# Optimization experiments

Hardware: AMD Instinct MI355X
Metric: run time of the kernel (lower is better)

Reference implementation:

```python
import jax, jax.numpy as jnp
import numpy as np

N_NODES = 100000
N_EDGES = 1600000
D_IN = 64
D_HID = 64
D_OUT = 64


def setup_inputs() -> dict:
    key = jax.random.key(0)
    ks = jax.random.split(key, 12)
    x = jax.random.normal(ks[0], (N_NODES, D_IN), dtype=jnp.float32)
    edge_index = jax.random.randint(ks[1], (2, N_EDGES), 0, N_NODES, dtype=jnp.int64)
    batch = jnp.zeros((N_NODES,), dtype=jnp.int64)
    # Glorot-ish init for GCNConv weights; PyG stores weight as [in, out] applied as x @ W.
    def lin(k, din, dout):
        s = 1.0 / np.sqrt(din)
        return jax.random.uniform(k, (din, dout), minval=-s, maxval=s, dtype=jnp.float32)
    W1 = lin(ks[2], D_IN, D_HID);  b1 = jnp.zeros((D_HID,), jnp.float32)
    W2 = lin(ks[3], D_HID, D_HID); b2 = jnp.zeros((D_HID,), jnp.float32)
    W3 = lin(ks[4], D_HID, D_HID); b3 = jnp.zeros((D_HID,), jnp.float32)
    W4 = lin(ks[5], D_HID, D_OUT); b4 = jnp.zeros((D_OUT,), jnp.float32)
    return {"x": x, "edge_index": edge_index, "batch": batch,
            "W1": W1, "b1": b1, "W2": W2, "b2": b2,
            "W3": W3, "b3": b3, "W4": W4, "b4": b4}


def reference(x, edge_index, batch, W1, b1, W2, b2, W3, b3, W4, b4):
    N = x.shape[0]
    loops = jnp.arange(N, dtype=edge_index.dtype)
    src = jnp.concatenate([edge_index[0], loops])  # [E+N]
    dst = jnp.concatenate([edge_index[1], loops])  # [E+N]
    # Symmetric normalization: deg over A + I (in-degree at dst), norm_e = d_src^-1/2 * d_dst^-1/2
    deg = jax.ops.segment_sum(jnp.ones(src.shape, dtype=x.dtype), dst, num_segments=N)
    dis = jnp.where(deg > 0, jax.lax.rsqrt(deg), 0.0)
    norm = (dis[src] * dis[dst])[:, None]  # [E+N, 1]

    def conv(h, W, b):
        h = h @ W                                   # [N, dout]
        msg = h[src] * norm                         # gather + scale, [E+N, dout]
        return jax.ops.segment_sum(msg, dst, num_segments=N) + b

    h = jax.nn.elu(conv(x, W1, b1))   # dropout_p=0.0 -> identity
    h = jax.nn.elu(conv(h, W2, b2))
    h = jax.nn.elu(conv(h, W3, b3))
    return conv(h, W4, b4)
```

## Files before the change

kernel.cpp:

```cpp
#include <hip/hip_runtime.h>

#define NN 100000
#define NE 1600000
#define DD 64
#define BSH 9
#define BSZ 512
#define NBKT 196
#define CHUNK 8192
#define NCH ((NE + CHUNK - 1) / CHUNK)
#define CSR2_CAP (NE + 16 * (NBKT * BSZ))


__global__ __launch_bounds__(256) void k_bcount(const int* __restrict__ ei,
                                                int* __restrict__ bcnt) {
    __shared__ int h[NBKT];
    int t = threadIdx.x;
    for (int i = t; i < NBKT; i += 256) h[i] = 0;
    __syncthreads();
    int base = blockIdx.x * CHUNK;
    for (int i = t; i < CHUNK; i += 256) {
        int e = base + i;
        if (e < NE) atomicAdd(&h[ei[NE + e] >> BSH], 1);
    }
    __syncthreads();
    for (int i = t; i < NBKT; i += 256)
        if (h[i]) atomicAdd(&bcnt[i], h[i]);
}


__global__ __launch_bounds__(256) void k_bscan(const int* __restrict__ bcnt,
                                               int* __restrict__ bbase,
                                               int* __restrict__ bcur) {
    __shared__ int s[256];
    int t = threadIdx.x;
    int v = (t < NBKT) ? bcnt[t] : 0;
    s[t] = v;
    __syncthreads();
    for (int o = 1; o < 256; o <<= 1) {
        int x = (t >= o) ? s[t - o] : 0;
        __syncthreads();
        s[t] += x;
        __syncthreads();
    }
    int ex = s[t] - v;
    if (t < NBKT) { bbase[t] = ex; bcur[t] = ex; }
    if (t == NBKT) bbase[NBKT] = ex;
}


__global__ __launch_bounds__(256) void k_bscat(const int* __restrict__ ei,
                                               int* __restrict__ bcur,
                                               int* __restrict__ bkt) {
    __shared__ int h[NBKT], rbase[NBKT], rcur[NBKT];
    int t = threadIdx.x;
    for (int i = t; i < NBKT; i += 256) h[i] = 0;
    __syncthreads();
    int cb = blockIdx.x * CHUNK;
    int s[32], d[32];
#pragma unroll
    for (int i = 0; i < 32; ++i) {
        int e = cb + t + 256 * i;
        if (e < NE) {
            s[i] = ei[e];
            d[i] = ei[NE + e];
            atomicAdd(&h[d[i] >> BSH], 1);
        } else {
            d[i] = -1;
        }
    }
    __syncthreads();
    for (int i = t; i < NBKT; i += 256) {
        int c = h[i];
        rbase[i] = c ? atomicAdd(&bcur[i], c) : 0;
        rcur[i] = 0;
    }
    __syncthreads();
#pragma unroll
    for (int i = 0; i < 32; ++i) {
        if (d[i] >= 0) {
            int b = d[i] >> BSH;
            int pos = rbase[b] + atomicAdd(&rcur[b], 1);
            bkt[pos] = s[i] | ((d[i] & (BSZ - 1)) << 17);
        }
    }
}


__global__ __launch_bounds__(256) void k_ncnt(const int* __restrict__ bbase,
                                              const int* __restrict__ bkt,
                                              int* __restrict__ ncnt,
                                              int* __restrict__ bptot,
                                              double* __restrict__ dis) {
    __shared__ int cnt[BSZ];
    __shared__ int red[256];
    int b = blockIdx.x, t = threadIdx.x;
    cnt[t] = 0; cnt[t + 256] = 0;
    __syncthreads();
    int beg = bbase[b], end = bbase[b + 1];
    for (int j = beg + t; j < end; j += 256)
        atomicAdd(&cnt[bkt[j] >> 17], 1);
    __syncthreads();
    int nb = b * BSZ;
    int n0 = nb + t, n1 = nb + t + 256;
    int c0 = cnt[t], c1 = cnt[t + 256];
    int p0 = (n0 < NN) ? ((c0 + 16) & ~15) : 0;
    int p1 = (n1 < NN) ? ((c1 + 16) & ~15) : 0;
    if (n0 < NN) { ncnt[n0] = c0; dis[n0] = 1.0 / sqrt((double)(c0 + 1)); }
    if (n1 < NN) { ncnt[n1] = c1; dis[n1] = 1.0 / sqrt((double)(c1 + 1)); }
    red[t] = p0 + p1;
    __syncthreads();
    for (int o = 128; o > 0; o >>= 1) {
        if (t < o) red[t] += red[t + o];
        __syncthreads();
    }
    if (t == 0) bptot[b] = red[0];
}


__global__ __launch_bounds__(256) void k_pscan(const int* __restrict__ bptot,
                                               int* __restrict__ pbase,
                                               int* __restrict__ rp2) {
    __shared__ int s[256];
    int t = threadIdx.x;
    int v = (t < NBKT) ? bptot[t] : 0;
    s[t] = v;
    __syncthreads();
    for (int o = 1; o < 256; o <<= 1) {
        int x = (t >= o) ? s[t - o] : 0;
        __syncthreads();
        s[t] += x;
        __syncthreads();
    }
    int ex = s[t] - v;
    if (t < NBKT) pbase[t] = ex;
    if (t == NBKT) rp2[NN] = ex;
}


__global__ __launch_bounds__(256) void k_bfill(const int* __restrict__ bbase,
                                               const int* __restrict__ bkt,
                                               const int* __restrict__ ncnt,
                                               const int* __restrict__ pbase,
                                               int* __restrict__ rp2,
                                               int* __restrict__ csr2) {
    __shared__ int cur[BSZ];
    __shared__ int s2[256];
    int b = blockIdx.x, t = threadIdx.x;
    int nb = b * BSZ;
    int gbase = pbase[b];
    int n0 = nb + 2 * t, n1 = nb + 2 * t + 1;
    int c0 = (n0 < NN) ? ncnt[n0] : -1;
    int c1 = (n1 < NN) ? ncnt[n1] : -1;
    int q0 = (c0 >= 0) ? ((c0 + 16) & ~15) : 0;
    int q1 = (c1 >= 0) ? ((c1 + 16) & ~15) : 0;
    s2[t] = q0 + q1;
    __syncthreads();
    for (int o = 1; o < 256; o <<= 1) {
        int v = (t >= o) ? s2[t - o] : 0;
        __syncthreads();
        s2[t] += v;
        __syncthreads();
    }
    int ex = s2[t] - (q0 + q1);
    if (c0 >= 0) { int g = gbase + ex;      rp2[n0] = g; csr2[g] = n0; cur[2 * t]     = ex + 1; }
    if (c1 >= 0) { int g = gbase + ex + q0; rp2[n1] = g; csr2[g] = n1; cur[2 * t + 1] = ex + q0 + 1; }
    __syncthreads();
    int beg = bbase[b], end = bbase[b + 1];
    for (int j = beg + t; j < end; j += 256) {
        int pk = bkt[j];
        int pos = gbase + atomicAdd(&cur[pk >> 17], 1);
        csr2[pos] = pk & 0x1FFFF;
    }
    __syncthreads();
    if (c0 >= 0) { int e0 = ex + q0;      for (int j = cur[2 * t];     j < e0; ++j) csr2[gbase + j] = NN; }
    if (c1 >= 0) { int e1 = ex + q0 + q1; for (int j = cur[2 * t + 1]; j < e1; ++j) csr2[gbase + j] = NN; }
}


__global__ __launch_bounds__(256) void k_gemm(const float* __restrict__ in,
                                              const float* __restrict__ W,
                                              const double* __restrict__ dis,
                                              float* __restrict__ h2s) {
    __shared__ float sW[DD * DD];
    __shared__ float sIn[128 * 65];
    int t = threadIdx.x;
    int brow = blockIdx.x * 128;
#pragma unroll
    for (int i = 0; i < 16; ++i) sW[t + 256 * i] = W[t + 256 * i];
#pragma unroll
    for (int i = 0; i < 32; ++i) {
        int idx = t + 256 * i;
        int rr = idx >> 6, kk = idx & 63;
        int gr = brow + rr; if (gr >= NN) gr = NN - 1;
        sIn[rr * 65 + kk] = in[(size_t)gr * DD + kk];
    }
    __syncthreads();
    int cg = t & 7;
    int rg = t >> 3;
    const float* sInB = &sIn[rg * 4 * 65];

    float aE[4][8], aO[4][8];
#pragma unroll
    for (int i = 0; i < 4; ++i)
#pragma unroll
        for (int j = 0; j < 8; ++j) { aE[i][j] = 0.f; aO[i][j] = 0.f; }

#pragma unroll 4
    for (int k = 0; k < DD; k += 2) {
        float4 w0 = *(const float4*)&sW[k * DD + cg * 8];
        float4 w1 = *(const float4*)&sW[k * DD + cg * 8 + 4];
        float4 w2 = *(const float4*)&sW[(k + 1) * DD + cg * 8];
        float4 w3 = *(const float4*)&sW[(k + 1) * DD + cg * 8 + 4];
        float wv0[8] = {w0.x, w0.y, w0.z, w0.w, w1.x, w1.y, w1.z, w1.w};
        float wv1[8] = {w2.x, w2.y, w2.z, w2.w, w3.x, w3.y, w3.z, w3.w};
#pragma unroll
        for (int i = 0; i < 4; ++i) {
            float a0 = sInB[i * 65 + k];
            float a1 = sInB[i * 65 + k + 1];
#pragma unroll
            for (int j = 0; j < 8; ++j) {
                aE[i][j] = fmaf(a0, wv0[j], aE[i][j]);
                aO[i][j] = fmaf(a1, wv1[j], aO[i][j]);
            }
        }
    }

#pragma unroll
    for (int i = 0; i < 4; ++i) {
        int row = brow + rg * 4 + i;
        if (row < NN) {
            double dr = dis[row];
            float o[8];
#pragma unroll
            for (int j = 0; j < 8; ++j)
                o[j] = (float)((double)(aE[i][j] + aO[i][j]) * dr);
            *(float4*)&h2s[(size_t)row * DD + cg * 8]     = make_float4(o[0], o[1], o[2], o[3]);
            *(float4*)&h2s[(size_t)row * DD + cg * 8 + 4] = make_float4(o[4], o[5], o[6], o[7]);
        }
    }
}


__global__ __launch_bounds__(256) void k_aggr(const int* __restrict__ rp2,
                                              const int* __restrict__ csr2,
                                              const float* __restrict__ h2s,
                                              const double* __restrict__ dis,
                                              const float* __restrict__ b,
                                              float* __restrict__ out,
                                              int apply_elu) {
    int gid = blockIdx.x * 256 + threadIdx.x;
    int node = gid >> 6;
    int lane = gid & 63;
    int beg = __builtin_amdgcn_readfirstlane(rp2[node]);
    int end = __builtin_amdgcn_readfirstlane(rp2[node + 1]);
    double a0 = 0.0, a1 = 0.0, a2 = 0.0, a3 = 0.0;
    for (int j = beg; j < end; j += 16) {
        int4 i0 = *(const int4*)&csr2[j];
        int4 i1 = *(const int4*)&csr2[j + 4];
        int4 i2 = *(const int4*)&csr2[j + 8];
        int4 i3 = *(const int4*)&csr2[j + 12];
        float v0  = h2s[(size_t)(unsigned)i0.x * DD + lane];
        float v1  = h2s[(size_t)(unsigned)i0.y * DD + lane];
        float v2  = h2s[(size_t)(unsigned)i0.z * DD + lane];
        float v3  = h2s[(size_t)(unsigned)i0.w * DD + lane];
        float v4  = h2s[(size_t)(unsigned)i1.x * DD + lane];
        float v5  = h2s[(size_t)(unsigned)i1.y * DD + lane];
        float v6  = h2s[(size_t)(unsigned)i1.z * DD + lane];
        float v7  = h2s[(size_t)(unsigned)i1.w * DD + lane];
        float v8  = h2s[(size_t)(unsigned)i2.x * DD + lane];
        float v9  = h2s[(size_t)(unsigned)i2.y * DD + lane];
        float v10 = h2s[(size_t)(unsigned)i2.z * DD + lane];
        float v11 = h2s[(size_t)(unsigned)i2.w * DD + lane];
        float v12 = h2s[(size_t)(unsigned)i3.x * DD + lane];
        float v13 = h2s[(size_t)(unsigned)i3.y * DD + lane];
        float v14 = h2s[(size_t)(unsigned)i3.z * DD + lane];
        float v15 = h2s[(size_t)(unsigned)i3.w * DD + lane];
        a0 += (double)v0;  a1 += (double)v1;  a2 += (double)v2;  a3 += (double)v3;
        a0 += (double)v4;  a1 += (double)v5;  a2 += (double)v6;  a3 += (double)v7;
        a0 += (double)v8;  a1 += (double)v9;  a2 += (double)v10; a3 += (double)v11;
        a0 += (double)v12; a1 += (double)v13; a2 += (double)v14; a3 += (double)v15;
    }
    double sum = (a0 + a1) + (a2 + a3);
    float vf = (float)(dis[node] * sum + (double)b[lane]);
    if (apply_elu && vf <= 0.f) vf = expm1f(vf);
    out[gid] = vf;
}


static inline size_t align256(size_t x) { return (x + 255) & ~(size_t)255; }

extern "C" void kernel_launch(void* const* d_in, const int* in_sizes, int n_in,
                              void* d_out, int out_size, void* d_ws, size_t ws_size,
                              hipStream_t stream) {
    const float* x  = (const float*)d_in[0];
    const int*   ei = (const int*)d_in[1];
    const float* W1 = (const float*)d_in[3];
    const float* b1 = (const float*)d_in[4];
    const float* W2 = (const float*)d_in[5];
    const float* b2 = (const float*)d_in[6];
    const float* W3 = (const float*)d_in[7];
    const float* b3 = (const float*)d_in[8];
    const float* W4 = (const float*)d_in[9];
    const float* b4 = (const float*)d_in[10];
    float* out = (float*)d_out;

    char* ws = (char*)d_ws;
    size_t off = 0;
    double* dis   = (double*)(ws + off); off = align256(off + (size_t)NN * sizeof(double));
    float*  h2s   = (float*) (ws + off); off = align256(off + (size_t)(NN + 1) * DD * sizeof(float));
    float*  A     = (float*) (ws + off); off = align256(off + (size_t)NN * DD * sizeof(float));
    int*    ncnt  = (int*)   (ws + off); off = align256(off + (size_t)NN * sizeof(int));
    int*    rp2   = (int*)   (ws + off); off = align256(off + (size_t)(NN + 1) * sizeof(int));
    int*    bcnt  = (int*)   (ws + off); off = align256(off + (size_t)(NBKT + 1) * sizeof(int));
    int*    bbase = (int*)   (ws + off); off = align256(off + (size_t)(NBKT + 1) * sizeof(int));
    int*    bcur  = (int*)   (ws + off); off = align256(off + (size_t)(NBKT + 1) * sizeof(int));
    int*    bptot = (int*)   (ws + off); off = align256(off + (size_t)(NBKT + 1) * sizeof(int));
    int*    pbase = (int*)   (ws + off); off = align256(off + (size_t)(NBKT + 1) * sizeof(int));
    int*    bkt   = (int*)   (ws + off); off = align256(off + (size_t)NE * sizeof(int));
    int*    csr2  = (int*)   (ws + off); off = align256(off + (size_t)CSR2_CAP * sizeof(int));

    hipMemsetAsync(bcnt, 0, (size_t)NBKT * sizeof(int), stream);
    hipMemsetAsync(h2s + (size_t)NN * DD, 0, DD * sizeof(float), stream);

    k_bcount<<<NCH, 256, 0, stream>>>(ei, bcnt);
    k_bscan<<<1, 256, 0, stream>>>(bcnt, bbase, bcur);
    k_bscat<<<NCH, 256, 0, stream>>>(ei, bcur, bkt);
    k_ncnt<<<NBKT, 256, 0, stream>>>(bbase, bkt, ncnt, bptot, dis);
    k_pscan<<<1, 256, 0, stream>>>(bptot, pbase, rp2);
    k_bfill<<<NBKT, 256, 0, stream>>>(bbase, bkt, ncnt, pbase, rp2, csr2);

    struct Layer { const float* in; const float* b; const float* W; float* o; int elu; };
    Layer L[4] = {
        { x,   b1, W1, A,   1 },
        { A,   b2, W2, out, 1 },
        { out, b3, W3, A,   1 },
        { A,   b4, W4, out, 0 },
    };

    for (int l = 0; l < 4; ++l) {
        k_gemm<<<(NN + 127) / 128, 256, 0, stream>>>(L[l].in, L[l].W, dis, h2s);
        k_aggr<<<NN / 4, 256, 0, stream>>>(rp2, csr2, h2s, dis, L[l].b, L[l].o, L[l].elu);
    }
}
```

Measured before the change: 386.9 us.

## Degree-sort nodes into sliced ELL groups with feature-sliced layout for aggregation

Nodes are reordered within each bucket by in-degree, grouped in eights, and stored in a sliced ELLPACK layout padded to each group's max degree. Features are split into eight 8-wide slices, so each aggregation block reads from one slice, which shrinks the gather working set and aims to improve cache hit rates. Intermediate activations stay in the permuted, sliced layout between layers, and the final layer scatters back to node-major order. This adds permutation kernels and padding overhead. Sliced loads in the gemm and a narrower 8-node-by-8-feature wave mapping may reduce coalescing.

Result: slower. 563.1 us (+45.5%).

```diff
diff --git a/kernel.cpp b/kernel.cpp
--- a/kernel.cpp
+++ b/kernel.cpp
@@ -8,7 +8,17 @@
 #define NBKT 196
 #define CHUNK 8192
 #define NCH ((NE + CHUNK - 1) / CHUNK)
-#define CSR2_CAP (NE + 16 * (NBKT * BSZ))
+#define NGRP (NN / 8)
+#define SLS ((size_t)(NN + 1) * 8)
+#define CSRT_CAP 4000000
+#define GPT 49
+
+
+__global__ void k_zero(int* __restrict__ bcnt, float* __restrict__ h2sS) {
+    int t = threadIdx.x;
+    if (t < NBKT) bcnt[t] = 0;
+    if (t < 64) h2sS[(size_t)(t >> 3) * SLS + (size_t)NN * 8 + (t & 7)] = 0.f;
+}
 
 
 __global__ __launch_bounds__(256) void k_bcount(const int* __restrict__ ei,
@@ -86,44 +96,85 @@
 }
 
 
-__global__ __launch_bounds__(256) void k_ncnt(const int* __restrict__ bbase,
+__global__ __launch_bounds__(256) void k_sort(const int* __restrict__ bbase,
                                               const int* __restrict__ bkt,
-                                              int* __restrict__ ncnt,
-                                              int* __restrict__ bptot,
-                                              double* __restrict__ dis) {
+                                              int* __restrict__ perm,
+                                              int* __restrict__ invp,
+                                              double* __restrict__ disP,
+                                              int* __restrict__ pdegP) {
     __shared__ int cnt[BSZ];
-    __shared__ int red[256];
+    __shared__ int bins[256], binb[256], bcur2[256];
     int b = blockIdx.x, t = threadIdx.x;
     cnt[t] = 0; cnt[t + 256] = 0;
+    bins[t] = 0;
     __syncthreads();
     int beg = bbase[b], end = bbase[b + 1];
     for (int j = beg + t; j < end; j += 256)
         atomicAdd(&cnt[bkt[j] >> 17], 1);
     __syncthreads();
     int nb = b * BSZ;
-    int n0 = nb + t, n1 = nb + t + 256;
-    int c0 = cnt[t], c1 = cnt[t + 256];
-    int p0 = (n0 < NN) ? ((c0 + 16) & ~15) : 0;
-    int p1 = (n1 < NN) ? ((c1 + 16) & ~15) : 0;
-    if (n0 < NN) { ncnt[n0] = c0; dis[n0] = 1.0 / sqrt((double)(c0 + 1)); }
-    if (n1 < NN) { ncnt[n1] = c1; dis[n1] = 1.0 / sqrt((double)(c1 + 1)); }
-    red[t] = p0 + p1;
-    __syncthreads();
-    for (int o = 128; o > 0; o >>= 1) {
-        if (t < o) red[t] += red[t + o];
-        __syncthreads();
-    }
-    if (t == 0) bptot[b] = red[0];
-}
-
-
-__global__ __launch_bounds__(256) void k_pscan(const int* __restrict__ bptot,
-                                               int* __restrict__ pbase,
-                                               int* __restrict__ rp2) {
+#pragma unroll
+    for (int u = 0; u < 2; ++u) {
+        int d = t + 256 * u;
+        if (nb + d < NN) atomicAdd(&bins[min(cnt[d], 255)], 1);
+    }
+    __syncthreads();
+    int v = bins[t];
+    binb[t] = v;
+    __syncthreads();
+    for (int o = 1; o < 256; o <<= 1) {
+        int x = (t >= o) ? binb[t - o] : 0;
+        __syncthreads();
+        binb[t] += x;
+        __syncthreads();
+    }
+    int ex = binb[t] - v;
+    __syncthreads();
+    binb[t] = ex;
+    bcur2[t] = 0;
+    __syncthreads();
+#pragma unroll
+    for (int u = 0; u < 2; ++u) {
+        int d = t + 256 * u;
+        int node = nb + d;
+        if (node < NN) {
+            int c = cnt[d];
+            int bin = min(c, 255);
+            int lr = binb[bin] + atomicAdd(&bcur2[bin], 1);
+            int r = nb + lr;
+            perm[r] = node;
+            invp[node] = r;
+            disP[r] = 1.0 / sqrt((double)(c + 1));
+            pdegP[r] = c + 1;
+        }
+    }
+}
+
+
+__global__ __launch_bounds__(256) void k_glen(const int* __restrict__ pdegP,
+                                              int* __restrict__ glen8) {
+    int g = blockIdx.x * 256 + threadIdx.x;
+    if (g < NGRP) {
+        int m = 0;
+#pragma unroll
+        for (int i = 0; i < 8; ++i) m = max(m, pdegP[g * 8 + i]);
+        int slots = (m + 3) & ~3;
+        glen8[g] = slots * 8;
+    }
+}
+
+
+__global__ __launch_bounds__(256) void k_gscan(const int* __restrict__ glen8,
+                                               int* __restrict__ gbase) {
     __shared__ int s[256];
     int t = threadIdx.x;
-    int v = (t < NBKT) ? bptot[t] : 0;
-    s[t] = v;
+    int base = t * GPT;
+    int sum = 0;
+    for (int i = 0; i < GPT; ++i) {
+        int g = base + i;
+        if (g < NGRP) sum += glen8[g];
+    }
+    s[t] = sum;
     __syncthreads();
     for (int o = 1; o < 256; o <<= 1) {
         int x = (t >= o) ? s[t - o] : 0;
@@ -131,68 +182,88 @@
         s[t] += x;
         __syncthreads();
     }
-    int ex = s[t] - v;
-    if (t < NBKT) pbase[t] = ex;
-    if (t == NBKT) rp2[NN] = ex;
-}
-
-
-__global__ __launch_bounds__(256) void k_bfill(const int* __restrict__ bbase,
-                                               const int* __restrict__ bkt,
-                                               const int* __restrict__ ncnt,
-                                               const int* __restrict__ pbase,
-                                               int* __restrict__ rp2,
-                                               int* __restrict__ csr2) {
+    int run = s[t] - sum;
+    for (int i = 0; i < GPT; ++i) {
+        int g = base + i;
+        if (g < NGRP) { gbase[g] = run; run += glen8[g]; }
+    }
+    if (t == 255) gbase[NGRP] = s[255];
+}
+
+
+__global__ __launch_bounds__(256) void k_ell(const int* __restrict__ bbase,
+                                             const int* __restrict__ bkt,
+                                             const int* __restrict__ invp,
+                                             const int* __restrict__ gbase,
+                                             int* __restrict__ csrT) {
     __shared__ int cur[BSZ];
-    __shared__ int s2[256];
+    __shared__ int eb8[BSZ];
+    __shared__ int gl[BSZ];
     int b = blockIdx.x, t = threadIdx.x;
     int nb = b * BSZ;
-    int gbase = pbase[b];
-    int n0 = nb + 2 * t, n1 = nb + 2 * t + 1;
-    int c0 = (n0 < NN) ? ncnt[n0] : -1;
-    int c1 = (n1 < NN) ? ncnt[n1] : -1;
-    int q0 = (c0 >= 0) ? ((c0 + 16) & ~15) : 0;
-    int q1 = (c1 >= 0) ? ((c1 + 16) & ~15) : 0;
-    s2[t] = q0 + q1;
-    __syncthreads();
-    for (int o = 1; o < 256; o <<= 1) {
-        int v = (t >= o) ? s2[t - o] : 0;
-        __syncthreads();
-        s2[t] += v;
-        __syncthreads();
-    }
-    int ex = s2[t] - (q0 + q1);
-    if (c0 >= 0) { int g = gbase + ex;      rp2[n0] = g; csr2[g] = n0; cur[2 * t]     = ex + 1; }
-    if (c1 >= 0) { int g = gbase + ex + q0; rp2[n1] = g; csr2[g] = n1; cur[2 * t + 1] = ex + q0 + 1; }
+#pragma unroll
+    for (int u = 0; u < 2; ++u) {
+        int d = t + 256 * u;
+        int node = nb + d;
+        if (node < NN) {
+            int r = invp[node];
+            int g = r >> 3;
+            int e0 = gbase[g];
+            int e = e0 + (r & 7);
+            eb8[d] = e;
+            gl[d] = (gbase[g + 1] - e0) >> 3;
+            csrT[e] = r;
+            cur[d] = 1;
+        }
+    }
     __syncthreads();
     int beg = bbase[b], end = bbase[b + 1];
     for (int j = beg + t; j < end; j += 256) {
         int pk = bkt[j];
-        int pos = gbase + atomicAdd(&cur[pk >> 17], 1);
-        csr2[pos] = pk & 0x1FFFF;
-    }
-    __syncthreads();
-    if (c0 >= 0) { int e0 = ex + q0;      for (int j = cur[2 * t];     j < e0; ++j) csr2[gbase + j] = NN; }
-    if (c1 >= 0) { int e1 = ex + q0 + q1; for (int j = cur[2 * t + 1]; j < e1; ++j) csr2[gbase + j] = NN; }
+        int dl = pk >> 17;
+        int sl = atomicAdd(&cur[dl], 1);
+        csrT[eb8[dl] + sl * 8] = invp[pk & 0x1FFFF];
+    }
+    __syncthreads();
+#pragma unroll
+    for (int u = 0; u < 2; ++u) {
+        int d = t + 256 * u;
+        if (nb + d < NN) {
+            int e = eb8[d];
+            int ge = gl[d];
+            for (int j = cur[d]; j < ge; ++j) csrT[e + j * 8] = NN;
+        }
+    }
 }
 
 
 __global__ __launch_bounds__(256) void k_gemm(const float* __restrict__ in,
+                                              const int* __restrict__ perm,
+                                              int sliced_in,
                                               const float* __restrict__ W,
-                                              const double* __restrict__ dis,
-                                              float* __restrict__ h2s) {
+                                              const double* __restrict__ disP,
+                                              float* __restrict__ h2sS) {
     __shared__ float sW[DD * DD];
     __shared__ float sIn[128 * 65];
+    __shared__ int sPerm[128];
     int t = threadIdx.x;
     int brow = blockIdx.x * 128;
+    if (!sliced_in && t < 128) sPerm[t] = perm[min(brow + t, NN - 1)];
 #pragma unroll
     for (int i = 0; i < 16; ++i) sW[t + 256 * i] = W[t + 256 * i];
+    __syncthreads();
 #pragma unroll
     for (int i = 0; i < 32; ++i) {
         int idx = t + 256 * i;
         int rr = idx >> 6, kk = idx & 63;
-        int gr = brow + rr; if (gr >= NN) gr = NN - 1;
-        sIn[rr * 65 + kk] = in[(size_t)gr * DD + kk];
+        float v;
+        if (sliced_in) {
+            int row = min(brow + rr, NN - 1);
+            v = in[(size_t)(kk >> 3) * SLS + (size_t)row * 8 + (kk & 7)];
+        } else {
+            v = in[(size_t)sPerm[rr] * DD + kk];
+        }
+        sIn[rr * 65 + kk] = v;
     }
     __syncthreads();
     int cg = t & 7;
@@ -229,61 +300,57 @@
     for (int i = 0; i < 4; ++i) {
         int row = brow + rg * 4 + i;
         if (row < NN) {
-            double dr = dis[row];
+            double dr = disP[row];
             float o[8];
 #pragma unroll
             for (int j = 0; j < 8; ++j)
                 o[j] = (float)((double)(aE[i][j] + aO[i][j]) * dr);
-            *(float4*)&h2s[(size_t)row * DD + cg * 8]     = make_float4(o[0], o[1], o[2], o[3]);
-            *(float4*)&h2s[(size_t)row * DD + cg * 8 + 4] = make_float4(o[4], o[5], o[6], o[7]);
-        }
-    }
-}
-
-
-__global__ __launch_bounds__(256) void k_aggr(const int* __restrict__ rp2,
-                                              const int* __restrict__ csr2,
-                                              const float* __restrict__ h2s,
-                                              const double* __restrict__ dis,
-                                              const float* __restrict__ b,
-                                              float* __restrict__ out,
-                                              int apply_elu) {
-    int gid = blockIdx.x * 256 + threadIdx.x;
-    int node = gid >> 6;
-    int lane = gid & 63;
-    int beg = __builtin_amdgcn_readfirstlane(rp2[node]);
-    int end = __builtin_amdgcn_readfirstlane(rp2[node + 1]);
-    double a0 = 0.0, a1 = 0.0, a2 = 0.0, a3 = 0.0;
-    for (int j = beg; j < end; j += 16) {
-        int4 i0 = *(const int4*)&csr2[j];
-        int4 i1 = *(const int4*)&csr2[j + 4];
-        int4 i2 = *(const int4*)&csr2[j + 8];
-        int4 i3 = *(const int4*)&csr2[j + 12];
-        float v0  = h2s[(size_t)(unsigned)i0.x * DD + lane];
-        float v1  = h2s[(size_t)(unsigned)i0.y * DD + lane];
-        float v2  = h2s[(size_t)(unsigned)i0.z * DD + lane];
-        float v3  = h2s[(size_t)(unsigned)i0.w * DD + lane];
-        float v4  = h2s[(size_t)(unsigned)i1.x * DD + lane];
-        float v5  = h2s[(size_t)(unsigned)i1.y * DD + lane];
-        float v6  = h2s[(size_t)(unsigned)i1.z * DD + lane];
-        float v7  = h2s[(size_t)(unsigned)i1.w * DD + lane];
-        float v8  = h2s[(size_t)(unsigned)i2.x * DD + lane];
-        float v9  = h2s[(size_t)(unsigned)i2.y * DD + lane];
-        float v10 = h2s[(size_t)(unsigned)i2.z * DD + lane];
-        float v11 = h2s[(size_t)(unsigned)i2.w * DD + lane];
-        float v12 = h2s[(size_t)(unsigned)i3.x * DD + lane];
-        float v13 = h2s[(size_t)(unsigned)i3.y * DD + lane];
-        float v14 = h2s[(size_t)(unsigned)i3.z * DD + lane];
-        float v15 = h2s[(size_t)(unsigned)i3.w * DD + lane];
-        a0 += (double)v0;  a1 += (double)v1;  a2 += (double)v2;  a3 += (double)v3;
-        a0 += (double)v4;  a1 += (double)v5;  a2 += (double)v6;  a3 += (double)v7;
-        a0 += (double)v8;  a1 += (double)v9;  a2 += (double)v10; a3 += (double)v11;
-        a0 += (double)v12; a1 += (double)v13; a2 += (double)v14; a3 += (double)v15;
-    }
-    double sum = (a0 + a1) + (a2 + a3);
-    float vf = (float)(dis[node] * sum + (double)b[lane]);
+            *(float4*)&h2sS[(size_t)cg * SLS + (size_t)row * 8]     = make_float4(o[0], o[1], o[2], o[3]);
+            *(float4*)&h2sS[(size_t)cg * SLS + (size_t)row * 8 + 4] = make_float4(o[4], o[5], o[6], o[7]);
+        }
+    }
+}
+
+
+__global__ __launch_bounds__(256) void k_aggr(const int* __restrict__ gbase,
+                                              const int* __restrict__ csrT,
+                                              const float* __restrict__ h2sS,
+                                              const double* __restrict__ disP,
+                                              const int* __restrict__ perm,
+                                              const float* __restrict__ bias,
+                                              float* __restrict__ outp,
+                                              int apply_elu, int out_node_major) {
+    int t = threadIdx.x;
+    int lane = t & 63;
+    int wid = __builtin_amdgcn_readfirstlane(t >> 6);
+    int s = blockIdx.x & 7;
+    int g = (blockIdx.x >> 3) * 4 + wid;
+    int n = lane >> 3, f = lane & 7;
+    int r = g * 8 + n;
+    int e0 = __builtin_amdgcn_readfirstlane(gbase[g]);
+    int e1 = __builtin_amdgcn_readfirstlane(gbase[g + 1]);
+    const float* sb = h2sS + (size_t)s * SLS;
+    double dn = disP[r];
+    float bv = bias[s * 8 + f];
+    double acc = 0.0;
+    for (int off = e0; off < e1; off += 32) {
+        int i0 = csrT[off + n];
+        int i1 = csrT[off + 8 + n];
+        int i2 = csrT[off + 16 + n];
+        int i3 = csrT[off + 24 + n];
+        float v0 = sb[(size_t)(unsigned)i0 * 8 + f];
+        float v1 = sb[(size_t)(unsigned)i1 * 8 + f];
+        float v2 = sb[(size_t)(unsigned)i2 * 8 + f];
+        float v3 = sb[(size_t)(unsigned)i3 * 8 + f];
+        acc += (double)v0;
+        acc += (double)v1;
+        acc += (double)v2;
+        acc += (double)v3;
+    }
+    float vf = (float)(dn * acc + (double)bv);
     if (apply_elu && vf <= 0.f) vf = expm1f(vf);
-    out[gid] = vf;
+    if (out_node_major) outp[(size_t)perm[r] * DD + s * 8 + f] = vf;
+    else                outp[(size_t)s * SLS + (size_t)r * 8 + f] = vf;
 }
 
 
@@ -306,39 +373,42 @@
 
     char* ws = (char*)d_ws;
     size_t off = 0;
-    double* dis   = (double*)(ws + off); off = align256(off + (size_t)NN * sizeof(double));
-    float*  h2s   = (float*) (ws + off); off = align256(off + (size_t)(NN + 1) * DD * sizeof(float));
-    float*  A     = (float*) (ws + off); off = align256(off + (size_t)NN * DD * sizeof(float));
-    int*    ncnt  = (int*)   (ws + off); off = align256(off + (size_t)NN * sizeof(int));
-    int*    rp2   = (int*)   (ws + off); off = align256(off + (size_t)(NN + 1) * sizeof(int));
+    float*  h2sS  = (float*) (ws + off); off = align256(off + 8 * SLS * sizeof(float));
+    float*  AS    = (float*) (ws + off); off = align256(off + 8 * SLS * sizeof(float));
+    double* disP  = (double*)(ws + off); off = align256(off + (size_t)NN * sizeof(double));
+    int*    perm  = (int*)   (ws + off); off = align256(off + (size_t)NN * sizeof(int));
+    int*    invp  = (int*)   (ws + off); off = align256(off + (size_t)NN * sizeof(int));
+    int*    pdegP = (int*)   (ws + off); off = align256(off + (size_t)NN * sizeof(int));
+    int*    glen8 = (int*)   (ws + off); off = align256(off + (size_t)NGRP * sizeof(int));
+    int*    gbase = (int*)   (ws + off); off = align256(off + (size_t)(NGRP + 1) * sizeof(int));
     int*    bcnt  = (int*)   (ws + off); off = align256(off + (size_t)(NBKT + 1) * sizeof(int));
     int*    bbase = (int*)   (ws + off); off = align256(off + (size_t)(NBKT + 1) * sizeof(int));
     int*    bcur  = (int*)   (ws + off); off = align256(off + (size_t)(NBKT + 1) * sizeof(int));
-    int*    bptot = (int*)   (ws + off); off = align256(off + (size_t)(NBKT + 1) * sizeof(int));
-    int*    pbase = (int*)   (ws + off); off = align256(off + (size_t)(NBKT + 1) * sizeof(int));
     int*    bkt   = (int*)   (ws + off); off = align256(off + (size_t)NE * sizeof(int));
-    int*    csr2  = (int*)   (ws + off); off = align256(off + (size_t)CSR2_CAP * sizeof(int));
-
-    hipMemsetAsync(bcnt, 0, (size_t)NBKT * sizeof(int), stream);
-    hipMemsetAsync(h2s + (size_t)NN * DD, 0, DD * sizeof(float), stream);
-
+    int*    csrT  = (int*)   (ws + off); off = align256(off + (size_t)CSRT_CAP * sizeof(int));
+
+    k_zero<<<1, 256, 0, stream>>>(bcnt, h2sS);
     k_bcount<<<NCH, 256, 0, stream>>>(ei, bcnt);
     k_bscan<<<1, 256, 0, stream>>>(bcnt, bbase, bcur);
     k_bscat<<<NCH, 256, 0, stream>>>(ei, bcur, bkt);
-    k_ncnt<<<NBKT, 256, 0, stream>>>(bbase, bkt, ncnt, bptot, dis);
-    k_pscan<<<1, 256, 0, stream>>>(bptot, pbase, rp2);
-    k_bfill<<<NBKT, 256, 0, stream>>>(bbase, bkt, ncnt, pbase, rp2, csr2);
-
-    struct Layer { const float* in; const float* b; const float* W; float* o; int elu; };
+    k_sort<<<NBKT, 256, 0, stream>>>(bbase, bkt, perm, invp, disP, pdegP);
+    k_glen<<<(NGRP + 255) / 256, 256, 0, stream>>>(pdegP, glen8);
+    k_gscan<<<1, 256, 0, stream>>>(glen8, gbase);
+    k_ell<<<NBKT, 256, 0, stream>>>(bbase, bkt, invp, gbase, csrT);
+
+    struct Layer { const float* in; int sliced; const float* W; const float* b;
+                   float* o; int elu; int nodemaj; };
     Layer L[4] = {
-        { x,   b1, W1, A,   1 },
-        { A,   b2, W2, out, 1 },
-        { out, b3, W3, A,   1 },
-        { A,   b4, W4, out, 0 },
+        { x,  0, W1, b1, AS,  1, 0 },
+        { AS, 1, W2, b2, AS,  1, 0 },
+        { AS, 1, W3, b3, AS,  1, 0 },
+        { AS, 1, W4, b4, out, 0, 1 },
     };
 
     for (int l = 0; l < 4; ++l) {
-        k_gemm<<<(NN + 127) / 128, 256, 0, stream>>>(L[l].in, L[l].W, dis, h2s);
-        k_aggr<<<NN / 4, 256, 0, stream>>>(rp2, csr2, h2s, dis, L[l].b, L[l].o, L[l].elu);
-    }
-}
+        k_gemm<<<(NN + 127) / 128, 256, 0, stream>>>(L[l].in, perm, L[l].sliced,
+                                                     L[l].W, disP, h2sS);
+        k_aggr<<<(NGRP / 4) * 8, 256, 0, stream>>>(gbase, csrT, h2sS, disP, perm,
+                                                   L[l].b, L[l].o, L[l].elu, L[l].nodemaj);
+    }
+}
```

## Renumber nodes by degree within buckets and shrink CSR row padding to 8

Applied to the files above, without the earlier changes.

Nodes are sorted by in-degree within each 512-node bucket with a counting sort. All intermediate layers run in this permuted order, the CSR holds permuted source ids, and the last aggregation scatters back to the original node order. The aim is to give the 4 wavefronts in each aggregation block similar row lengths so they finish together. Rows are now padded to multiples of 8 with an 8-wide tail instead of 16, which cuts wasted padding gathers. A single zeroing kernel replaces two memsets. The cost is extra permutation indirection in the first GEMM load and the final store, plus more setup work.

Measured after the change: 448.4 us. +15.9%, slower.

```diff
diff --git a/kernel.cpp b/kernel.cpp
--- a/kernel.cpp
+++ b/kernel.cpp
@@ -8,7 +8,14 @@
 #define NBKT 196
 #define CHUNK 8192
 #define NCH ((NE + CHUNK - 1) / CHUNK)
-#define CSR2_CAP (NE + 16 * (NBKT * BSZ))
+#define CSR2_CAP (NE + 8 * NN + 64)
+
+
+__global__ void k_zero(int* __restrict__ bcnt, float* __restrict__ h2s) {
+    int t = threadIdx.x;
+    if (t < NBKT) bcnt[t] = 0;
+    if (t < DD) h2s[(size_t)NN * DD + t] = 0.f;
+}
 
 
 __global__ __launch_bounds__(256) void k_bcount(const int* __restrict__ ei,
@@ -86,28 +93,64 @@
 }
 
 
-__global__ __launch_bounds__(256) void k_ncnt(const int* __restrict__ bbase,
+__global__ __launch_bounds__(256) void k_sort(const int* __restrict__ bbase,
                                               const int* __restrict__ bkt,
-                                              int* __restrict__ ncnt,
-                                              int* __restrict__ bptot,
-                                              double* __restrict__ dis) {
+                                              int* __restrict__ perm,
+                                              int* __restrict__ invp,
+                                              double* __restrict__ disP,
+                                              int* __restrict__ pdegP,
+                                              int* __restrict__ bptot) {
     __shared__ int cnt[BSZ];
-    __shared__ int red[256];
+    __shared__ int bins[256], binb[256], bcur2[256], red[256];
     int b = blockIdx.x, t = threadIdx.x;
     cnt[t] = 0; cnt[t + 256] = 0;
+    bins[t] = 0;
     __syncthreads();
     int beg = bbase[b], end = bbase[b + 1];
     for (int j = beg + t; j < end; j += 256)
         atomicAdd(&cnt[bkt[j] >> 17], 1);
     __syncthreads();
     int nb = b * BSZ;
-    int n0 = nb + t, n1 = nb + t + 256;
-    int c0 = cnt[t], c1 = cnt[t + 256];
-    int p0 = (n0 < NN) ? ((c0 + 16) & ~15) : 0;
-    int p1 = (n1 < NN) ? ((c1 + 16) & ~15) : 0;
-    if (n0 < NN) { ncnt[n0] = c0; dis[n0] = 1.0 / sqrt((double)(c0 + 1)); }
-    if (n1 < NN) { ncnt[n1] = c1; dis[n1] = 1.0 / sqrt((double)(c1 + 1)); }
-    red[t] = p0 + p1;
+    int padsum = 0;
+#pragma unroll
+    for (int u = 0; u < 2; ++u) {
+        int d = t + 256 * u;
+        if (nb + d < NN) {
+            atomicAdd(&bins[min(cnt[d], 255)], 1);
+            padsum += (cnt[d] + 8) & ~7;
+        }
+    }
+    red[t] = padsum;
+    __syncthreads();
+    int v = bins[t];
+    binb[t] = v;
+    __syncthreads();
+    for (int o = 1; o < 256; o <<= 1) {
+        int x = (t >= o) ? binb[t - o] : 0;
+        __syncthreads();
+        binb[t] += x;
+        __syncthreads();
+    }
+    int ex = binb[t] - v;
+    __syncthreads();
+    binb[t] = ex;
+    bcur2[t] = 0;
+    __syncthreads();
+#pragma unroll
+    for (int u = 0; u < 2; ++u) {
+        int d = t + 256 * u;
+        int node = nb + d;
+        if (node < NN) {
+            int c = cnt[d];
+            int bin = min(c, 255);
+            int lr = binb[bin] + atomicAdd(&bcur2[bin], 1);
+            int r = nb + lr;
+            perm[r] = node;
+            invp[node] = r;
+            disP[r] = 1.0 / sqrt((double)(c + 1));
+            pdegP[r] = c + 1;
+        }
+    }
     __syncthreads();
     for (int o = 128; o > 0; o >>= 1) {
         if (t < o) red[t] += red[t + o];
@@ -139,20 +182,27 @@
 
 __global__ __launch_bounds__(256) void k_bfill(const int* __restrict__ bbase,
                                                const int* __restrict__ bkt,
-                                               const int* __restrict__ ncnt,
+                                               const int* __restrict__ pdegP,
                                                const int* __restrict__ pbase,
+                                               const int* __restrict__ invp,
                                                int* __restrict__ rp2,
                                                int* __restrict__ csr2) {
     __shared__ int cur[BSZ];
+    __shared__ int lrOf[BSZ];
     __shared__ int s2[256];
     int b = blockIdx.x, t = threadIdx.x;
     int nb = b * BSZ;
     int gbase = pbase[b];
-    int n0 = nb + 2 * t, n1 = nb + 2 * t + 1;
-    int c0 = (n0 < NN) ? ncnt[n0] : -1;
-    int c1 = (n1 < NN) ? ncnt[n1] : -1;
-    int q0 = (c0 >= 0) ? ((c0 + 16) & ~15) : 0;
-    int q1 = (c1 >= 0) ? ((c1 + 16) & ~15) : 0;
+#pragma unroll
+    for (int u = 0; u < 2; ++u) {
+        int d = t + 256 * u;
+        if (nb + d < NN) lrOf[d] = invp[nb + d] - nb;
+    }
+    int r0 = nb + 2 * t, r1 = nb + 2 * t + 1;
+    int p0 = (r0 < NN) ? pdegP[r0] : -1;
+    int p1 = (r1 < NN) ? pdegP[r1] : -1;
+    int q0 = (p0 >= 0) ? ((p0 + 7) & ~7) : 0;
+    int q1 = (p1 >= 0) ? ((p1 + 7) & ~7) : 0;
     s2[t] = q0 + q1;
     __syncthreads();
     for (int o = 1; o < 256; o <<= 1) {
@@ -162,37 +212,49 @@
         __syncthreads();
     }
     int ex = s2[t] - (q0 + q1);
-    if (c0 >= 0) { int g = gbase + ex;      rp2[n0] = g; csr2[g] = n0; cur[2 * t]     = ex + 1; }
-    if (c1 >= 0) { int g = gbase + ex + q0; rp2[n1] = g; csr2[g] = n1; cur[2 * t + 1] = ex + q0 + 1; }
+    if (p0 >= 0) { int g = gbase + ex;      rp2[r0] = g; csr2[g] = r0; cur[2 * t]     = ex + 1; }
+    if (p1 >= 0) { int g = gbase + ex + q0; rp2[r1] = g; csr2[g] = r1; cur[2 * t + 1] = ex + q0 + 1; }
     __syncthreads();
     int beg = bbase[b], end = bbase[b + 1];
     for (int j = beg + t; j < end; j += 256) {
         int pk = bkt[j];
-        int pos = gbase + atomicAdd(&cur[pk >> 17], 1);
-        csr2[pos] = pk & 0x1FFFF;
-    }
-    __syncthreads();
-    if (c0 >= 0) { int e0 = ex + q0;      for (int j = cur[2 * t];     j < e0; ++j) csr2[gbase + j] = NN; }
-    if (c1 >= 0) { int e1 = ex + q0 + q1; for (int j = cur[2 * t + 1]; j < e1; ++j) csr2[gbase + j] = NN; }
+        int lr = lrOf[pk >> 17];
+        int pos = gbase + atomicAdd(&cur[lr], 1);
+        csr2[pos] = invp[pk & 0x1FFFF];
+    }
+    __syncthreads();
+    if (p0 >= 0) { int e0 = ex + q0;      for (int j = cur[2 * t];     j < e0; ++j) csr2[gbase + j] = NN; }
+    if (p1 >= 0) { int e1 = ex + q0 + q1; for (int j = cur[2 * t + 1]; j < e1; ++j) csr2[gbase + j] = NN; }
 }
 
 
 __global__ __launch_bounds__(256) void k_gemm(const float* __restrict__ in,
+                                              const int* __restrict__ perm,
+                                              int permuted_in,
                                               const float* __restrict__ W,
-                                              const double* __restrict__ dis,
+                                              const double* __restrict__ disP,
                                               float* __restrict__ h2s) {
     __shared__ float sW[DD * DD];
     __shared__ float sIn[128 * 65];
+    __shared__ int sPerm[128];
     int t = threadIdx.x;
     int brow = blockIdx.x * 128;
+    if (permuted_in && t < 128) sPerm[t] = perm[min(brow + t, NN - 1)];
 #pragma unroll
     for (int i = 0; i < 16; ++i) sW[t + 256 * i] = W[t + 256 * i];
+    __syncthreads();
 #pragma unroll
     for (int i = 0; i < 32; ++i) {
         int idx = t + 256 * i;
         int rr = idx >> 6, kk = idx & 63;
-        int gr = brow + rr; if (gr >= NN) gr = NN - 1;
-        sIn[rr * 65 + kk] = in[(size_t)gr * DD + kk];
+        float v;
+        if (permuted_in) {
+            v = in[(size_t)sPerm[rr] * DD + kk];
+        } else {
+            int row = min(brow + rr, NN - 1);
+            v = in[(size_t)row * DD + kk];
+        }
+        sIn[rr * 65 + kk] = v;
     }
     __syncthreads();
     int cg = t & 7;
@@ -229,7 +291,7 @@
     for (int i = 0; i < 4; ++i) {
         int row = brow + rg * 4 + i;
         if (row < NN) {
-            double dr = dis[row];
+            double dr = disP[row];
             float o[8];
 #pragma unroll
             for (int j = 0; j < 8; ++j)
@@ -244,17 +306,19 @@
 __global__ __launch_bounds__(256) void k_aggr(const int* __restrict__ rp2,
                                               const int* __restrict__ csr2,
                                               const float* __restrict__ h2s,
-                                              const double* __restrict__ dis,
-                                              const float* __restrict__ b,
-                                              float* __restrict__ out,
-                                              int apply_elu) {
+                                              const double* __restrict__ disP,
+                                              const int* __restrict__ perm,
+                                              const float* __restrict__ bias,
+                                              float* __restrict__ outp,
+                                              int apply_elu, int out_node_major) {
     int gid = blockIdx.x * 256 + threadIdx.x;
-    int node = gid >> 6;
+    int r = gid >> 6;
     int lane = gid & 63;
-    int beg = __builtin_amdgcn_readfirstlane(rp2[node]);
-    int end = __builtin_amdgcn_readfirstlane(rp2[node + 1]);
+    int beg = __builtin_amdgcn_readfirstlane(rp2[r]);
+    int end = __builtin_amdgcn_readfirstlane(rp2[r + 1]);
     double a0 = 0.0, a1 = 0.0, a2 = 0.0, a3 = 0.0;
-    for (int j = beg; j < end; j += 16) {
+    int j = beg;
+    for (; j + 16 <= end; j += 16) {
         int4 i0 = *(const int4*)&csr2[j];
         int4 i1 = *(const int4*)&csr2[j + 4];
         int4 i2 = *(const int4*)&csr2[j + 8];
@@ -280,10 +344,29 @@
         a0 += (double)v8;  a1 += (double)v9;  a2 += (double)v10; a3 += (double)v11;
         a0 += (double)v12; a1 += (double)v13; a2 += (double)v14; a3 += (double)v15;
     }
+    if (j < end) {
+        int4 i0 = *(const int4*)&csr2[j];
+        int4 i1 = *(const int4*)&csr2[j + 4];
+        float v0 = h2s[(size_t)(unsigned)i0.x * DD + lane];
+        float v1 = h2s[(size_t)(unsigned)i0.y * DD + lane];
+        float v2 = h2s[(size_t)(unsigned)i0.z * DD + lane];
+        float v3 = h2s[(size_t)(unsigned)i0.w * DD + lane];
+        float v4 = h2s[(size_t)(unsigned)i1.x * DD + lane];
+        float v5 = h2s[(size_t)(unsigned)i1.y * DD + lane];
+        float v6 = h2s[(size_t)(unsigned)i1.z * DD + lane];
+        float v7 = h2s[(size_t)(unsigned)i1.w * DD + lane];
+        a0 += (double)v0; a1 += (double)v1; a2 += (double)v2; a3 += (double)v3;
+        a0 += (double)v4; a1 += (double)v5; a2 += (double)v6; a3 += (double)v7;
+    }
     double sum = (a0 + a1) + (a2 + a3);
-    float vf = (float)(dis[node] * sum + (double)b[lane]);
+    float vf = (float)(disP[r] * sum + (double)bias[lane]);
     if (apply_elu && vf <= 0.f) vf = expm1f(vf);
-    out[gid] = vf;
+    if (out_node_major) {
+        int node = __builtin_amdgcn_readfirstlane(perm[r]);
+        outp[(size_t)node * DD + lane] = vf;
+    } else {
+        outp[(size_t)r * DD + lane] = vf;
+    }
 }
 
 
@@ -306,10 +389,12 @@
 
     char* ws = (char*)d_ws;
     size_t off = 0;
-    double* dis   = (double*)(ws + off); off = align256(off + (size_t)NN * sizeof(double));
     float*  h2s   = (float*) (ws + off); off = align256(off + (size_t)(NN + 1) * DD * sizeof(float));
     float*  A     = (float*) (ws + off); off = align256(off + (size_t)NN * DD * sizeof(float));
-    int*    ncnt  = (int*)   (ws + off); off = align256(off + (size_t)NN * sizeof(int));
+    double* disP  = (double*)(ws + off); off = align256(off + (size_t)NN * sizeof(double));
+    int*    perm  = (int*)   (ws + off); off = align256(off + (size_t)NN * sizeof(int));
+    int*    invp  = (int*)   (ws + off); off = align256(off + (size_t)NN * sizeof(int));
+    int*    pdegP = (int*)   (ws + off); off = align256(off + (size_t)NN * sizeof(int));
     int*    rp2   = (int*)   (ws + off); off = align256(off + (size_t)(NN + 1) * sizeof(int));
     int*    bcnt  = (int*)   (ws + off); off = align256(off + (size_t)(NBKT + 1) * sizeof(int));
     int*    bbase = (int*)   (ws + off); off = align256(off + (size_t)(NBKT + 1) * sizeof(int));
@@ -319,26 +404,27 @@
     int*    bkt   = (int*)   (ws + off); off = align256(off + (size_t)NE * sizeof(int));
     int*    csr2  = (int*)   (ws + off); off = align256(off + (size_t)CSR2_CAP * sizeof(int));
 
-    hipMemsetAsync(bcnt, 0, (size_t)NBKT * sizeof(int), stream);
-    hipMemsetAsync(h2s + (size_t)NN * DD, 0, DD * sizeof(float), stream);
-
+    k_zero<<<1, 256, 0, stream>>>(bcnt, h2s);
     k_bcount<<<NCH, 256, 0, stream>>>(ei, bcnt);
     k_bscan<<<1, 256, 0, stream>>>(bcnt, bbase, bcur);
     k_bscat<<<NCH, 256, 0, stream>>>(ei, bcur, bkt);
-    k_ncnt<<<NBKT, 256, 0, stream>>>(bbase, bkt, ncnt, bptot, dis);
+    k_sort<<<NBKT, 256, 0, stream>>>(bbase, bkt, perm, invp, disP, pdegP, bptot);
     k_pscan<<<1, 256, 0, stream>>>(bptot, pbase, rp2);
-    k_bfill<<<NBKT, 256, 0, stream>>>(bbase, bkt, ncnt, pbase, rp2, csr2);
-
-    struct Layer { const float* in; const float* b; const float* W; float* o; int elu; };
+    k_bfill<<<NBKT, 256, 0, stream>>>(bbase, bkt, pdegP, pbase, invp, rp2, csr2);
+
+    struct Layer { const float* in; int permuted; const float* W; const float* b;
+                   float* o; int elu; int nodemaj; };
     Layer L[4] = {
-        { x,   b1, W1, A,   1 },
-        { A,   b2, W2, out, 1 },
-        { out, b3, W3, A,   1 },
-        { A,   b4, W4, out, 0 },
+        { x, 1, W1, b1, A,   1, 0 },
+        { A, 0, W2, b2, A,   1, 0 },
+        { A, 0, W3, b3, A,   1, 0 },
+        { A, 0, W4, b4, out, 0, 1 },
     };
 
     for (int l = 0; l < 4; ++l) {
-        k_gemm<<<(NN + 127) / 128, 256, 0, stream>>>(L[l].in, L[l].W, dis, h2s);
-        k_aggr<<<NN / 4, 256, 0, stream>>>(rp2, csr2, h2s, dis, L[l].b, L[l].o, L[l].elu);
-    }
-}
+        k_gemm<<<(NN + 127) / 128, 256, 0, stream>>>(L[l].in, perm, L[l].permuted,
+                                                     L[l].W, disP, h2s);
+        k_aggr<<<NN / 4, 256, 0, stream>>>(rp2, csr2, h2s, disP, perm,
+                                           L[l].b, L[l].o, L[l].elu, L[l].nodemaj);
+    }
+}
```

## Fuse aggregation+ELU of each layer into the next layer's GEMM kernel

Applied to the files above, without the earlier changes.

Adds a k_fused kernel in which each block gathers neighbour sums for 128 nodes, applies bias and ELU, writes the result into shared memory and then runs the next layer's 64x64 GEMM on that tile. The intermediate activation round trip through global memory disappears, and the launch count drops from eight to five. The GEMM output now alternates between two ping-pong h2s buffers, and the two memsets become one small zeroing kernel. The trade-off is parallelism for the latency-bound gather: each wave now handles 32 nodes one after another, and the large LDS footprint limits how many blocks fit on a CU.

Result: slower. 534.4 us (+38.1%).

```diff
diff --git a/kernel.cpp b/kernel.cpp
--- a/kernel.cpp
+++ b/kernel.cpp
@@ -8,7 +8,16 @@
 #define NBKT 196
 #define CHUNK 8192
 #define NCH ((NE + CHUNK - 1) / CHUNK)
-#define CSR2_CAP (NE + 16 * (NBKT * BSZ))
+#define CSR2_CAP (NE + 16 * NN + 1024)
+
+
+__global__ void k_zero(int* __restrict__ bcnt,
+                       float* __restrict__ h2sA, float* __restrict__ h2sB) {
+    int t = threadIdx.x;
+    if (t < NBKT) bcnt[t] = 0;
+    if (t < DD) h2sA[(size_t)NN * DD + t] = 0.f;
+    if (t >= 64 && t < 128) h2sB[(size_t)NN * DD + (t - 64)] = 0.f;
+}
 
 
 __global__ __launch_bounds__(256) void k_bcount(const int* __restrict__ ei,
@@ -177,24 +186,8 @@
 }
 
 
-__global__ __launch_bounds__(256) void k_gemm(const float* __restrict__ in,
-                                              const float* __restrict__ W,
-                                              const double* __restrict__ dis,
-                                              float* __restrict__ h2s) {
-    __shared__ float sW[DD * DD];
-    __shared__ float sIn[128 * 65];
-    int t = threadIdx.x;
-    int brow = blockIdx.x * 128;
-#pragma unroll
-    for (int i = 0; i < 16; ++i) sW[t + 256 * i] = W[t + 256 * i];
-#pragma unroll
-    for (int i = 0; i < 32; ++i) {
-        int idx = t + 256 * i;
-        int rr = idx >> 6, kk = idx & 63;
-        int gr = brow + rr; if (gr >= NN) gr = NN - 1;
-        sIn[rr * 65 + kk] = in[(size_t)gr * DD + kk];
-    }
-    __syncthreads();
+__device__ __forceinline__ void gemm_phase(const float* sW, const float* sIn,
+                                           const double* dis, float* h2s, int brow, int t) {
     int cg = t & 7;
     int rg = t >> 3;
     const float* sInB = &sIn[rg * 4 * 65];
@@ -241,13 +234,92 @@
 }
 
 
+__global__ __launch_bounds__(256) void k_gemm(const float* __restrict__ in,
+                                              const float* __restrict__ W,
+                                              const double* __restrict__ dis,
+                                              float* __restrict__ h2s) {
+    __shared__ float sW[DD * DD];
+    __shared__ float sIn[128 * 65];
+    int t = threadIdx.x;
+    int brow = blockIdx.x * 128;
+#pragma unroll
+    for (int i = 0; i < 16; ++i) sW[t + 256 * i] = W[t + 256 * i];
+#pragma unroll
+    for (int i = 0; i < 32; ++i) {
+        int idx = t + 256 * i;
+        int rr = idx >> 6, kk = idx & 63;
+        int gr = brow + rr; if (gr >= NN) gr = NN - 1;
+        sIn[rr * 65 + kk] = in[(size_t)gr * DD + kk];
+    }
+    __syncthreads();
+    gemm_phase(sW, sIn, dis, h2s, brow, t);
+}
+
+
+__global__ __launch_bounds__(256) void k_fused(const int* __restrict__ rp2,
+                                               const int* __restrict__ csr2,
+                                               const float* __restrict__ h2s_old,
+                                               const double* __restrict__ dis,
+                                               const float* __restrict__ bias,
+                                               const float* __restrict__ W,
+                                               float* __restrict__ h2s_new) {
+    __shared__ float sW[DD * DD];
+    __shared__ float sIn[128 * 65];
+    int t = threadIdx.x;
+    int brow = blockIdx.x * 128;
+#pragma unroll
+    for (int i = 0; i < 16; ++i) sW[t + 256 * i] = W[t + 256 * i];
+
+    int lane = t & 63;
+    int w = t >> 6;
+    float bv = bias[lane];
+    for (int rr = w * 32; rr < w * 32 + 32; ++rr) {
+        int r = brow + rr;
+        if (r >= NN) { sIn[rr * 65 + lane] = 0.f; continue; }
+        int beg = __builtin_amdgcn_readfirstlane(rp2[r]);
+        int end = __builtin_amdgcn_readfirstlane(rp2[r + 1]);
+        double a0 = 0.0, a1 = 0.0, a2 = 0.0, a3 = 0.0;
+        for (int j = beg; j < end; j += 16) {
+            int4 i0 = *(const int4*)&csr2[j];
+            int4 i1 = *(const int4*)&csr2[j + 4];
+            int4 i2 = *(const int4*)&csr2[j + 8];
+            int4 i3 = *(const int4*)&csr2[j + 12];
+            float v0  = h2s_old[(size_t)(unsigned)i0.x * DD + lane];
+            float v1  = h2s_old[(size_t)(unsigned)i0.y * DD + lane];
+            float v2  = h2s_old[(size_t)(unsigned)i0.z * DD + lane];
+            float v3  = h2s_old[(size_t)(unsigned)i0.w * DD + lane];
+            float v4  = h2s_old[(size_t)(unsigned)i1.x * DD + lane];
+            float v5  = h2s_old[(size_t)(unsigned)i1.y * DD + lane];
+            float v6  = h2s_old[(size_t)(unsigned)i1.z * DD + lane];
+            float v7  = h2s_old[(size_t)(unsigned)i1.w * DD + lane];
+            float v8  = h2s_old[(size_t)(unsigned)i2.x * DD + lane];
+            float v9  = h2s_old[(size_t)(unsigned)i2.y * DD + lane];
+            float v10 = h2s_old[(size_t)(unsigned)i2.z * DD + lane];
+            float v11 = h2s_old[(size_t)(unsigned)i2.w * DD + lane];
+            float v12 = h2s_old[(size_t)(unsigned)i3.x * DD + lane];
+            float v13 = h2s_old[(size_t)(unsigned)i3.y * DD + lane];
+            float v14 = h2s_old[(size_t)(unsigned)i3.z * DD + lane];
+            float v15 = h2s_old[(size_t)(unsigned)i3.w * DD + lane];
+            a0 += (double)v0;  a1 += (double)v1;  a2 += (double)v2;  a3 += (double)v3;
+            a0 += (double)v4;  a1 += (double)v5;  a2 += (double)v6;  a3 += (double)v7;
+            a0 += (double)v8;  a1 += (double)v9;  a2 += (double)v10; a3 += (double)v11;
+            a0 += (double)v12; a1 += (double)v13; a2 += (double)v14; a3 += (double)v15;
+        }
+        float vf = (float)(dis[r] * ((a0 + a1) + (a2 + a3)) + (double)bv);
+        if (vf <= 0.f) vf = expm1f(vf);
+        sIn[rr * 65 + lane] = vf;
+    }
+    __syncthreads();
+    gemm_phase(sW, sIn, dis, h2s_new, brow, t);
+}
+
+
 __global__ __launch_bounds__(256) void k_aggr(const int* __restrict__ rp2,
                                               const int* __restrict__ csr2,
                                               const float* __restrict__ h2s,
                                               const double* __restrict__ dis,
                                               const float* __restrict__ b,
-                                              float* __restrict__ out,
-                                              int apply_elu) {
+                                              float* __restrict__ out) {
     int gid = blockIdx.x * 256 + threadIdx.x;
     int node = gid >> 6;
     int lane = gid & 63;
@@ -281,9 +353,7 @@
         a0 += (double)v12; a1 += (double)v13; a2 += (double)v14; a3 += (double)v15;
     }
     double sum = (a0 + a1) + (a2 + a3);
-    float vf = (float)(dis[node] * sum + (double)b[lane]);
-    if (apply_elu && vf <= 0.f) vf = expm1f(vf);
-    out[gid] = vf;
+    out[gid] = (float)(dis[node] * sum + (double)b[lane]);
 }
 
 
@@ -306,9 +376,9 @@
 
     char* ws = (char*)d_ws;
     size_t off = 0;
+    float*  h2sA  = (float*) (ws + off); off = align256(off + (size_t)(NN + 1) * DD * sizeof(float));
+    float*  h2sB  = (float*) (ws + off); off = align256(off + (size_t)(NN + 1) * DD * sizeof(float));
     double* dis   = (double*)(ws + off); off = align256(off + (size_t)NN * sizeof(double));
-    float*  h2s   = (float*) (ws + off); off = align256(off + (size_t)(NN + 1) * DD * sizeof(float));
-    float*  A     = (float*) (ws + off); off = align256(off + (size_t)NN * DD * sizeof(float));
     int*    ncnt  = (int*)   (ws + off); off = align256(off + (size_t)NN * sizeof(int));
     int*    rp2   = (int*)   (ws + off); off = align256(off + (size_t)(NN + 1) * sizeof(int));
     int*    bcnt  = (int*)   (ws + off); off = align256(off + (size_t)(NBKT + 1) * sizeof(int));
@@ -319,9 +389,7 @@
     int*    bkt   = (int*)   (ws + off); off = align256(off + (size_t)NE * sizeof(int));
     int*    csr2  = (int*)   (ws + off); off = align256(off + (size_t)CSR2_CAP * sizeof(int));
 
-    hipMemsetAsync(bcnt, 0, (size_t)NBKT * sizeof(int), stream);
-    hipMemsetAsync(h2s + (size_t)NN * DD, 0, DD * sizeof(float), stream);
-
+    k_zero<<<1, 256, 0, stream>>>(bcnt, h2sA, h2sB);
     k_bcount<<<NCH, 256, 0, stream>>>(ei, bcnt);
     k_bscan<<<1, 256, 0, stream>>>(bcnt, bbase, bcur);
     k_bscat<<<NCH, 256, 0, stream>>>(ei, bcur, bkt);
@@ -329,16 +397,10 @@
     k_pscan<<<1, 256, 0, stream>>>(bptot, pbase, rp2);
     k_bfill<<<NBKT, 256, 0, stream>>>(bbase, bkt, ncnt, pbase, rp2, csr2);
 
-    struct Layer { const float* in; const float* b; const float* W; float* o; int elu; };
-    Layer L[4] = {
-        { x,   b1, W1, A,   1 },
-        { A,   b2, W2, out, 1 },
-        { out, b3, W3, A,   1 },
-        { A,   b4, W4, out, 0 },
-    };
-
-    for (int l = 0; l < 4; ++l) {
-        k_gemm<<<(NN + 127) / 128, 256, 0, stream>>>(L[l].in, L[l].W, dis, h2s);
-        k_aggr<<<NN / 4, 256, 0, stream>>>(rp2, csr2, h2s, dis, L[l].b, L[l].o, L[l].elu);
-    }
-}
+    const int NGB = (NN + 127) / 128;
+    k_gemm <<<NGB, 256, 0, stream>>>(x, W1, dis, h2sA);
+    k_fused<<<NGB, 256, 0, stream>>>(rp2, csr2, h2sA, dis, b1, W2, h2sB);
+    k_fused<<<NGB, 256, 0, stream>>>(rp2, csr2, h2sB, dis, b2, W3, h2sA);
+    k_fused<<<NGB, 256, 0, stream>>>(rp2, csr2, h2sA, dis, b3, W4, h2sB);
+    k_aggr <<<NN / 4, 256, 0, stream>>>(rp2, csr2, h2sB, dis, b4, out);
+}
```
